# Kernel optimization log

Hardware: AMD Instinct MI355X
Metric: run time of the kernel (lower is better)

## Reference

```python
import jax, jax.numpy as jnp
import numpy as np

NEG_SLOPE = 0.2  # GATv2Conv default leaky_relu slope

def _ln(x, g, b, eps=1e-5):
    mu = jnp.mean(x, -1, keepdims=True)
    v = jnp.mean((x - mu) ** 2, -1, keepdims=True)
    return (x - mu) / jnp.sqrt(v + eps) * g + b

def _seg_softmax(s, seg, n):
    m = jax.ops.segment_max(s, seg, n)
    m = jnp.where(jnp.isfinite(m), m, 0.0)  # guard empty segments
    e = jnp.exp(s - m[seg])
    z = jax.ops.segment_sum(e, seg, n)
    return e / (z[seg] + 1e-16)

def _gatv2(x, src, dst, Wl, bl, Wr, br, att, bias, g, b):
    # GATv2Conv (concat=True) + dropout(noop, eval) + residual (dims match) + LN + ELU
    N = x.shape[0]
    H, D = att.shape
    xl = (x @ Wl + bl).reshape(N, H, D)   # source transform
    xr = (x @ Wr + br).reshape(N, H, D)   # target transform
    e = jax.nn.leaky_relu(xl[src] + xr[dst], NEG_SLOPE)  # [E,H,D]
    sc = jnp.einsum('ehd,hd->eh', e, att)
    alpha = _seg_softmax(sc, dst, N)      # softmax over incoming edges per dst
    out = jax.ops.segment_sum(alpha[..., None] * xl[src], dst, N).reshape(N, H * D) + bias
    out = out + x                          # residual: in_dim == heads*out_dim
    return jax.nn.elu(_ln(out, g, b))

def _lstm(x, w_ih, w_hh, b_ih, b_hh):
    # torch LSTM gate order: i, f, g, o
    Hn = w_hh.shape[1]
    def step(carry, xt):
        h, c = carry
        gates = xt @ w_ih.T + h @ w_hh.T + b_ih + b_hh
        i, f, gg, o = jnp.split(gates, 4, -1)
        c = jax.nn.sigmoid(f) * c + jax.nn.sigmoid(i) * jnp.tanh(gg)
        h = jax.nn.sigmoid(o) * jnp.tanh(c)
        return (h, c), h
    h0 = jnp.zeros((x.shape[0], Hn), x.dtype)
    _, hs = jax.lax.scan(step, (h0, h0), jnp.swapaxes(x, 0, 1))
    return jnp.swapaxes(hs, 0, 1)  # [N,T,Hn]

def setup_inputs():
    key = jax.random.key(0)
    N, T, F, Hd, Hh, L = 20000, 20, 64, 256, 4, 2
    E, S, ES = 640000, 64, 1024
    D = Hd // Hh
    ks = iter(jax.random.split(key, 90))
    def nrm(shape, scale):
        return jax.random.normal(next(ks), shape, jnp.float32) * scale
    sH = Hd ** -0.5
    inp = {}
    inp['x_stock'] = nrm((N, T, F), 1.0)
    inp['edge_index_stock'] = jax.random.randint(next(ks), (2, E), 0, N)
    inp['batch_stock'] = jnp.sort(jax.random.randint(next(ks), (N,), 0, S))
    inp['x_sector'] = nrm((S, Hd), 1.0)
    inp['edge_index_sector'] = jax.random.randint(next(ks), (2, ES), 0, S)
    inp['ln_feat_g'] = jnp.ones(F); inp['ln_feat_b'] = jnp.zeros(F)
    inp['w_ih0'] = nrm((4 * Hd, F), F ** -0.5); inp['w_hh0'] = nrm((4 * Hd, Hd), sH)
    inp['b_ih0'] = jnp.zeros(4 * Hd); inp['b_hh0'] = jnp.zeros(4 * Hd)
    inp['w_ih1'] = nrm((4 * Hd, Hd), sH); inp['w_hh1'] = nrm((4 * Hd, Hd), sH)
    inp['b_ih1'] = jnp.zeros(4 * Hd); inp['b_hh1'] = jnp.zeros(4 * Hd)
    inp['ln_t_g'] = jnp.ones(Hd); inp['ln_t_b'] = jnp.zeros(Hd)
    inp['W_in'] = nrm((Hd, Hd), sH); inp['b_in'] = jnp.zeros(Hd)
    for p in ('stock', 'sector'):
        inp[p + '_Wl'] = nrm((L, Hd, Hd), sH); inp[p + '_bl'] = jnp.zeros((L, Hd))
        inp[p + '_Wr'] = nrm((L, Hd, Hd), sH); inp[p + '_br'] = jnp.zeros((L, Hd))
        inp[p + '_att'] = nrm((L, Hh, D), sH); inp[p + '_bias'] = jnp.zeros((L, Hd))
        inp[p + '_g'] = jnp.ones((L, Hd)); inp[p + '_b'] = jnp.zeros((L, Hd))
    inp['Wa1'] = nrm((Hd, Hd // 2), sH); inp['ba1'] = jnp.zeros(Hd // 2)
    inp['Wa2'] = nrm((Hd // 2, 1), (Hd // 2) ** -0.5); inp['ba2'] = jnp.zeros(1)
    inp['Wf'] = nrm((2 * Hd, Hd), (2 * Hd) ** -0.5); inp['bf'] = jnp.zeros(Hd)
    inp['gf'] = jnp.ones(Hd); inp['bef'] = jnp.zeros(Hd)
    for t in ('regf', 'clff', 'rnkf'):
        inp['W_' + t] = nrm((Hd, Hd), sH); inp['b_' + t] = jnp.zeros(Hd)
        inp['g_' + t] = jnp.ones(Hd); inp['be_' + t] = jnp.zeros(Hd)
    h2, h4 = Hd // 2, Hd // 4
    inp['Wr1'] = nrm((Hd, h2), sH); inp['br1'] = jnp.zeros(h2)
    inp['Wr2'] = nrm((h2, h4), h2 ** -0.5); inp['br2'] = jnp.zeros(h4)
    inp['Wr3'] = nrm((h4, 1), h4 ** -0.5); inp['br3'] = jnp.zeros(1)
    inp['Wc1'] = nrm((Hd, h2), sH); inp['bc1'] = jnp.zeros(h2)
    inp['Wc2'] = nrm((h2, 2), h2 ** -0.5); inp['bc2'] = jnp.zeros(2)
    inp['Wk1'] = nrm((Hd, h2), sH); inp['bk1'] = jnp.zeros(h2)
    inp['Wk2'] = nrm((h2, 1), h2 ** -0.5); inp['bk2'] = jnp.zeros(1)
    return inp

def _forward(x_stock, x_sector, ln_feat_g, ln_feat_b, w_ih0, w_hh0, b_ih0, b_hh0,
             w_ih1, w_hh1, b_ih1, b_hh1, ln_t_g, ln_t_b, W_in, b_in,
             stock_Wl, stock_bl, stock_Wr, stock_br, stock_att, stock_bias, stock_g, stock_b,
             Wa1, ba1, Wa2, ba2,
             sector_Wl, sector_bl, sector_Wr, sector_br, sector_att, sector_bias, sector_g, sector_b,
             Wf, bf, gf, bef,
             W_regf, b_regf, g_regf, be_regf, W_clff, b_clff, g_clff, be_clff,
             W_rnkf, b_rnkf, g_rnkf, be_rnkf,
             Wr1, br1, Wr2, br2, Wr3, br3, Wc1, bc1, Wc2, bc2, Wk1, bk1, Wk2, bk2,
             edge_index_stock, batch_stock, edge_index_sector):
    N = x_stock.shape[0]
    S = x_sector.shape[0]  # x_sector is otherwise unused by the torch forward
    # feature_norm + 2-layer LSTM temporal encoder (eval mode: dropout off)
    x = _ln(x_stock, ln_feat_g, ln_feat_b)
    h = _lstm(x, w_ih0, w_hh0, b_ih0, b_hh0)
    h = _lstm(h, w_ih1, w_hh1, b_ih1, b_hh1)
    x = _ln(h[:, -1], ln_t_g, ln_t_b)
    x = x @ W_in + b_in
    # stock GAT stack (with self loops, as in add_self_loops=True)
    sl = jnp.arange(N)
    src = jnp.concatenate([edge_index_stock[0], sl])
    dst = jnp.concatenate([edge_index_stock[1], sl])
    for l in range(stock_Wl.shape[0]):
        x = _gatv2(x, src, dst, stock_Wl[l], stock_bl[l], stock_Wr[l], stock_br[l],
                   stock_att[l], stock_bias[l], stock_g[l], stock_b[l])
    # attention pooling: per-sector softmax then mean pool of weighted feats
    sc = (jnp.tanh(x @ Wa1 + ba1) @ Wa2 + ba2)[:, 0]
    w = _seg_softmax(sc, batch_stock, S)
    cnt = jax.ops.segment_sum(jnp.ones(N, x.dtype), batch_stock, S)
    se = jax.ops.segment_sum(w[:, None] * x, batch_stock, S) / jnp.maximum(cnt, 1.0)[:, None]
    # sector GAT stack
    ssl = jnp.arange(S)
    ssrc = jnp.concatenate([edge_index_sector[0], ssl])
    sdst = jnp.concatenate([edge_index_sector[1], ssl])
    for l in range(sector_Wl.shape[0]):
        se = _gatv2(se, ssrc, sdst, sector_Wl[l], sector_bl[l], sector_Wr[l], sector_br[l],
                    sector_att[l], sector_bias[l], sector_g[l], sector_b[l])
    comb = jnp.concatenate([x, se[batch_stock]], -1)
    c = jax.nn.elu(_ln(comb @ Wf + bf, gf, bef))  # fusion_proj
    rf = jax.nn.relu(_ln(c @ W_regf + b_regf, g_regf, be_regf))
    cf = jax.nn.relu(_ln(c @ W_clff + b_clff, g_clff, be_clff))
    kf = jax.nn.relu(_ln(c @ W_rnkf + b_rnkf, g_rnkf, be_rnkf))
    ret = jnp.tanh(jax.nn.relu(jax.nn.relu(rf @ Wr1 + br1) @ Wr2 + br2) @ Wr3 + br3)[:, 0] * 0.1
    mov = jax.nn.relu(cf @ Wc1 + bc1) @ Wc2 + bc2
    rnk = jax.nn.sigmoid(jax.nn.relu(kf @ Wk1 + bk1) @ Wk2 + bk2)[:, 0]
    return ret, mov, rnk, c

def reference(x_stock, x_sector, ln_feat_g, ln_feat_b, w_ih0, w_hh0, b_ih0, b_hh0,
              w_ih1, w_hh1, b_ih1, b_hh1, ln_t_g, ln_t_b, W_in, b_in,
              stock_Wl, stock_bl, stock_Wr, stock_br, stock_att, stock_bias, stock_g, stock_b,
              Wa1, ba1, Wa2, ba2,
              sector_Wl, sector_bl, sector_Wr, sector_br, sector_att, sector_bias, sector_g, sector_b,
              Wf, bf, gf, bef,
              W_regf, b_regf, g_regf, be_regf, W_clff, b_clff, g_clff, be_clff,
              W_rnkf, b_rnkf, g_rnkf, be_rnkf,
              Wr1, br1, Wr2, br2, Wr3, br3, Wc1, bc1, Wc2, bc2, Wk1, bk1, Wk2, bk2,
              edge_index_stock, batch_stock, edge_index_sector):
    return _forward(x_stock, x_sector, ln_feat_g, ln_feat_b, w_ih0, w_hh0, b_ih0, b_hh0,
                    w_ih1, w_hh1, b_ih1, b_hh1, ln_t_g, ln_t_b, W_in, b_in,
                    stock_Wl, stock_bl, stock_Wr, stock_br, stock_att, stock_bias, stock_g, stock_b,
                    Wa1, ba1, Wa2, ba2,
                    sector_Wl, sector_bl, sector_Wr, sector_br, sector_att, sector_bias, sector_g, sector_b,
                    Wf, bf, gf, bef,
                    W_regf, b_regf, g_regf, be_regf, W_clff, b_clff, g_clff, be_clff,
                    W_rnkf, b_rnkf, g_rnkf, be_rnkf,
                    Wr1, br1, Wr2, br2, Wr3, br3, Wc1, bc1, Wc2, bc2, Wk1, bk1, Wk2, bk2,
                    edge_index_stock, batch_stock, edge_index_sector)
```

## Files before the change

kernel.cpp:

```cpp
#include <hip/hip_runtime.h>
#include <stdint.h>

static constexpr int TT = 20;
static constexpr int FF = 64;
static constexpr int HD = 256;

enum { ACT_NONE = 0, ACT_RELU = 1, ACT_TANH = 2 };

typedef __attribute__((ext_vector_type(8))) short short8;
typedef __attribute__((ext_vector_type(4))) float f32x4;

static __device__ __forceinline__ float sigf(float x) { return 1.f / (1.f + expf(-x)); }

static __device__ __forceinline__ ushort f2bf(float f) {
  uint32_t u = __float_as_uint(f);
  return (ushort)((u + 0x7fffu + ((u >> 16) & 1u)) >> 16);
}
static __device__ __forceinline__ float bf2f(ushort u) {
  return __uint_as_float(((uint32_t)u) << 16);
}
static __device__ __forceinline__ void gl16(const void* g, void* l) {
  __builtin_amdgcn_global_load_lds(
      (const __attribute__((address_space(1))) uint32_t*)g,
      (__attribute__((address_space(3))) uint32_t*)l, 16, 0, 0);
}

__global__ void k_lncvt(const float* __restrict__ x, const float* __restrict__ g,
                        const float* __restrict__ b, ushort* __restrict__ y, int rows) {
  int row = blockIdx.x * 4 + (threadIdx.x >> 6);
  int lane = threadIdx.x & 63;
  if (row >= rows) return;
  float v = x[(size_t)row * 64 + lane];
  float s = v, s2 = v * v;
  for (int o = 32; o; o >>= 1) { s += __shfl_xor(s, o); s2 += __shfl_xor(s2, o); }
  float m = s * (1.f / 64.f);
  float var = s2 * (1.f / 64.f) - m * m;
  float rs = rsqrtf(var + 1e-5f);
  y[(size_t)row * 64 + lane] = f2bf((v - m) * rs * g[lane] + b[lane]);
}

__global__ void k_build_wtile(const float* __restrict__ w_ih, const float* __restrict__ w_hh,
                              ushort* __restrict__ wt, int KI, int KT) {
  int total = 8 * KT * 512;
  for (int idx = blockIdx.x * blockDim.x + threadIdx.x; idx < total;
       idx += gridDim.x * blockDim.x) {
    int nb = idx / (KT * 512);
    int rem = idx % (KT * 512);
    int kt = rem / 512;
    int q = rem % 512;
    int r = q >> 2, csw = q & 3;
    int ch = csw ^ ((r >> 1) & 3);
    int col = nb * 128 + r;
    int hdblk = col >> 6, gg = (col >> 4) & 3, hd = hdblk * 16 + (col & 15);
    int orow = gg * HD + hd;
    int k = kt * 32 + ch * 8;
    const float* src = (k < KI) ? (w_ih + (size_t)orow * KI + k)
                                : (w_hh + (size_t)orow * HD + (k - KI));
    ushort* dst = wt + (size_t)idx * 8;
#pragma unroll
    for (int j = 0; j < 8; j++) dst[j] = f2bf(src[j]);
  }
}

__global__ void k_build_bcp(const float* __restrict__ bi, const float* __restrict__ bh,
                            float* __restrict__ bcp) {
  int col = blockIdx.x * blockDim.x + threadIdx.x;
  if (col >= 1024) return;
  int hdblk = col >> 6, gg = (col >> 4) & 3, hd = hdblk * 16 + (col & 15);
  int orow = gg * HD + hd;
  bcp[col] = bi[orow] + bh[orow];
}

__global__ void k_build_btile(const float* __restrict__ B, ushort* __restrict__ bt,
                              int K, int Nn, int NB) {
  int KTb = K / 32;
  int total = NB * KTb * 512;
  for (int idx = blockIdx.x * blockDim.x + threadIdx.x; idx < total;
       idx += gridDim.x * blockDim.x) {
    int nb = idx / (KTb * 512);
    int rem = idx % (KTb * 512);
    int kt = rem / 512;
    int q = rem % 512;
    int r = q >> 2, csw = q & 3;
    int ch = csw ^ ((r >> 1) & 3);
    int col = nb * 128 + r;
    int k = kt * 32 + ch * 8;
    ushort* dst = bt + (size_t)idx * 8;
#pragma unroll
    for (int j = 0; j < 8; j++)
      dst[j] = (col < Nn) ? f2bf(B[(size_t)(k + j) * Nn + col]) : (ushort)0;
  }
}

__global__ void k_cat2(const float* __restrict__ a, const float* __restrict__ b,
                       float* __restrict__ o) {
  int i = blockIdx.x * 256 + threadIdx.x;
  if (i < 256) o[i] = a[i];
  else if (i < 512) o[i] = b[i - 256];
}

template <int LAYER>
__device__ __forceinline__ void lstm_body(
    ushort* At, ushort* Bt,
    const ushort* __restrict__ a0, const ushort* __restrict__ a1,
    const ushort* __restrict__ wt, const float* __restrict__ bcp,
    float* __restrict__ cst, ushort* __restrict__ hnext, int M, int t) {
  constexpr int K = (LAYER == 0) ? 320 : 512;
  constexpr int KT = K / 32;
  constexpr int SEG0 = (LAYER == 0) ? 64 : 256;
  constexpr int LDA0 = (LAYER == 0) ? (TT * FF) : HD;
  const int tid = threadIdx.x;
  const int lane = tid & 63, wid = tid >> 6;
  const int wr = wid >> 1, wc = wid & 1;
  const int m0 = blockIdx.x * 128;
  const int nb = blockIdx.y;
  const int a0t = (LAYER == 0) ? t * FF : 0;

  f32x4 acc[4][4];
#pragma unroll
  for (int i = 0; i < 4; i++)
#pragma unroll
    for (int j = 0; j < 4; j++) acc[i][j] = (f32x4){0.f, 0.f, 0.f, 0.f};

  int rown[2], chn[2];
#pragma unroll
  for (int e = 0; e < 2; e++) {
    int q = e * 256 + tid;
    int r = q >> 2, csw = q & 3;
    rown[e] = r;
    chn[e] = csw ^ ((r >> 1) & 3);
  }
  const size_t wtbase = (size_t)nb * KT * 512;

  for (int kt = 0; kt < KT; ++kt) {
    __syncthreads();
    const int k0 = kt * 32;
#pragma unroll
    for (int e = 0; e < 2; e++) {
      int q = e * 256 + tid;
      int r = rown[e];
      int kg = k0 + chn[e] * 8;
      int grow = m0 + r;
      grow = (grow < M) ? grow : (M - 1);
      const ushort* src = (kg < SEG0)
                              ? (a0 + (size_t)grow * LDA0 + a0t + kg)
                              : (a1 + (size_t)grow * HD + (kg - SEG0));
      gl16(src, &At[q * 8]);
      gl16(wt + (wtbase + (size_t)kt * 512 + q) * 8, &Bt[q * 8]);
    }
    __syncthreads();
    short8 af[4], bfr[4];
#pragma unroll
    for (int i = 0; i < 4; i++) {
      int rA = wr * 64 + i * 16 + (lane & 15);
      int swa = (lane >> 4) ^ ((rA >> 1) & 3);
      af[i] = *(const short8*)&At[rA * 32 + swa * 8];
      int rB = wc * 64 + i * 16 + (lane & 15);
      int swb = (lane >> 4) ^ ((rB >> 1) & 3);
      bfr[i] = *(const short8*)&Bt[rB * 32 + swb * 8];
    }
#pragma unroll
    for (int i = 0; i < 4; i++)
#pragma unroll
      for (int j = 0; j < 4; j++)
        acc[i][j] = __builtin_amdgcn_mfma_f32_16x16x32_bf16(af[i], bfr[j], acc[i][j], 0, 0, 0);
  }
  const int hdlo = lane & 15;
  const int rb = (lane >> 4) * 4;
  const int colb = nb * 128 + wc * 64;
  const float bI = bcp[colb + hdlo];
  const float bF = bcp[colb + 16 + hdlo];
  const float bG = bcp[colb + 32 + hdlo];
  const float bO = bcp[colb + 48 + hdlo];
  const int hd = (nb * 2 + wc) * 16 + hdlo;
#pragma unroll
  for (int i = 0; i < 4; i++) {
#pragma unroll
    for (int r = 0; r < 4; r++) {
      int row = m0 + wr * 64 + i * 16 + rb + r;
      if (row >= M) continue;
      float gi = acc[i][0][r] + bI;
      float gf = acc[i][1][r] + bF;
      float gg = acc[i][2][r] + bG;
      float go = acc[i][3][r] + bO;
      size_t ix = (size_t)row * HD + hd;
      float c = sigf(gf) * cst[ix] + sigf(gi) * tanhf(gg);
      cst[ix] = c;
      hnext[ix] = f2bf(sigf(go) * tanhf(c));
    }
  }
}

template <int LAYER>
__global__ __launch_bounds__(256) void k_lstm_single(
    const ushort* __restrict__ a0, const ushort* __restrict__ a1,
    const ushort* __restrict__ wt, const float* __restrict__ bcp,
    float* __restrict__ cst, ushort* __restrict__ hnext, int M, int t) {
  __shared__ ushort At[128 * 32];
  __shared__ ushort Bt[128 * 32];
  lstm_body<LAYER>(At, Bt, a0, a1, wt, bcp, cst, hnext, M, t);
}

__global__ __launch_bounds__(256) void k_lstm_pair(
    const ushort* __restrict__ xln,
    const ushort* __restrict__ h0cur, const ushort* __restrict__ h1cur,
    const ushort* __restrict__ wt0, const float* __restrict__ bcp0,
    const ushort* __restrict__ wt1, const float* __restrict__ bcp1,
    float* __restrict__ c0, float* __restrict__ c1,
    ushort* __restrict__ h0next, ushort* __restrict__ h1next,
    int M, int tnext) {
  __shared__ ushort At[128 * 32];
  __shared__ ushort Bt[128 * 32];
  if (blockIdx.z == 0)
    lstm_body<1>(At, Bt, h0cur, h1cur, wt1, bcp1, c1, h1next, M, 0);
  else
    lstm_body<0>(At, Bt, xln, h0cur, wt0, bcp0, c0, h0next, M, tnext);
}

template <bool BF16OUT>
__global__ __launch_bounds__(256) void k_gemm_mfma(
    const float* __restrict__ A, int lda, const ushort* __restrict__ BtG,
    const float* __restrict__ bias, void* __restrict__ Cv, int ldc,
    int M, int Nn, int K, int act) {
  const int KTb = K / 32;
  __shared__ ushort At[128 * 32];
  __shared__ ushort Bts[128 * 32];
  const int tid = threadIdx.x;
  const int lane = tid & 63, wid = tid >> 6;
  const int wr = wid >> 1, wc = wid & 1;
  const int m0 = blockIdx.x * 128;
  const int nb = blockIdx.y;

  f32x4 acc[4][4];
#pragma unroll
  for (int i = 0; i < 4; i++)
#pragma unroll
    for (int j = 0; j < 4; j++) acc[i][j] = (f32x4){0.f, 0.f, 0.f, 0.f};

  const size_t btbase = (size_t)nb * KTb * 512;

  for (int kt = 0; kt < KTb; ++kt) {
    __syncthreads();
    const int k0 = kt * 32;
#pragma unroll
    for (int e = 0; e < 2; e++) {
      int q = e * 256 + tid;
      int r = q >> 2, csw = q & 3;
      int ch = csw ^ ((r >> 1) & 3);
      int row = m0 + r;
      row = (row < M) ? row : (M - 1);
      const float* src = A + (size_t)row * lda + k0 + ch * 8;
      float4 f0 = *(const float4*)src;
      float4 f1 = *(const float4*)(src + 4);
      short8 s;
      s[0] = (short)f2bf(f0.x); s[1] = (short)f2bf(f0.y);
      s[2] = (short)f2bf(f0.z); s[3] = (short)f2bf(f0.w);
      s[4] = (short)f2bf(f1.x); s[5] = (short)f2bf(f1.y);
      s[6] = (short)f2bf(f1.z); s[7] = (short)f2bf(f1.w);
      *(short8*)&At[q * 8] = s;
      gl16(BtG + (btbase + (size_t)kt * 512 + q) * 8, &Bts[q * 8]);
    }
    __syncthreads();
    short8 af[4], bfr[4];
#pragma unroll
    for (int i = 0; i < 4; i++) {
      int rA = wr * 64 + i * 16 + (lane & 15);
      int swa = (lane >> 4) ^ ((rA >> 1) & 3);
      af[i] = *(const short8*)&At[rA * 32 + swa * 8];
      int rB = wc * 64 + i * 16 + (lane & 15);
      int swb = (lane >> 4) ^ ((rB >> 1) & 3);
      bfr[i] = *(const short8*)&Bts[rB * 32 + swb * 8];
    }
#pragma unroll
    for (int i = 0; i < 4; i++)
#pragma unroll
      for (int j = 0; j < 4; j++)
        acc[i][j] = __builtin_amdgcn_mfma_f32_16x16x32_bf16(af[i], bfr[j], acc[i][j], 0, 0, 0);
  }
  const int rb = (lane >> 4) * 4;
  const int cl = lane & 15;
#pragma unroll
  for (int i = 0; i < 4; i++) {
#pragma unroll
    for (int j = 0; j < 4; j++) {
      int col = nb * 128 + wc * 64 + j * 16 + cl;
      if (col >= Nn) continue;
      float bv = bias[col];
#pragma unroll
      for (int r = 0; r < 4; r++) {
        int row = m0 + wr * 64 + i * 16 + rb + r;
        if (row >= M) continue;
        float v = acc[i][j][r] + bv;
        if (act == ACT_RELU) v = fmaxf(v, 0.f);
        else if (act == ACT_TANH) v = tanhf(v);
        if (BF16OUT) ((ushort*)Cv)[(size_t)row * ldc + col] = f2bf(v);
        else ((float*)Cv)[(size_t)row * ldc + col] = v;
      }
    }
  }
}

__global__ __launch_bounds__(256) void k_ln_rows(
    const float* __restrict__ in, float* __restrict__ out,
    const float* __restrict__ g, const float* __restrict__ b, int rows, int act) {
  int row = blockIdx.x;
  if (row >= rows) return;
  int tid = threadIdx.x, lane = tid & 63, wv = tid >> 6;
  float v = in[(size_t)row * HD + tid];
  float s = v, s2 = v * v;
  for (int o = 32; o; o >>= 1) { s += __shfl_xor(s, o); s2 += __shfl_xor(s2, o); }
  __shared__ float ws1[4], ws2[4];
  if (lane == 0) { ws1[wv] = s; ws2[wv] = s2; }
  __syncthreads();
  float S1 = ws1[0] + ws1[1] + ws1[2] + ws1[3];
  float S2 = ws2[0] + ws2[1] + ws2[2] + ws2[3];
  float m = S1 * (1.f / 256.f);
  float var = S2 * (1.f / 256.f) - m * m;
  float r = rsqrtf(var + 1e-5f);
  float y = (v - m) * r * g[tid] + b[tid];
  if (act == 1) y = fmaxf(y, 0.f);
  else if (act == 2) y = (y > 0.f) ? y : (expf(y) - 1.f);
  out[(size_t)row * HD + tid] = y;
}

__global__ __launch_bounds__(256) void k_ln_rows_b16(
    const ushort* __restrict__ in, float* __restrict__ out,
    const float* __restrict__ g, const float* __restrict__ b, int rows, int act) {
  int row = blockIdx.x;
  if (row >= rows) return;
  int tid = threadIdx.x, lane = tid & 63, wv = tid >> 6;
  float v = bf2f(in[(size_t)row * HD + tid]);
  float s = v, s2 = v * v;
  for (int o = 32; o; o >>= 1) { s += __shfl_xor(s, o); s2 += __shfl_xor(s2, o); }
  __shared__ float ws1[4], ws2[4];
  if (lane == 0) { ws1[wv] = s; ws2[wv] = s2; }
  __syncthreads();
  float S1 = ws1[0] + ws1[1] + ws1[2] + ws1[3];
  float S2 = ws2[0] + ws2[1] + ws2[2] + ws2[3];
  float m = S1 * (1.f / 256.f);
  float var = S2 * (1.f / 256.f) - m * m;
  float r = rsqrtf(var + 1e-5f);
  float y = (v - m) * r * g[tid] + b[tid];
  if (act == 1) y = fmaxf(y, 0.f);
  else if (act == 2) y = (y > 0.f) ? y : (expf(y) - 1.f);
  out[(size_t)row * HD + tid] = y;
}

__global__ void k_hist_edges(const int* __restrict__ dst, int E, int n, int* __restrict__ cnt) {
  int tot = E + n;
  for (int i = blockIdx.x * blockDim.x + threadIdx.x; i < tot; i += gridDim.x * blockDim.x) {
    int d = (i < E) ? dst[i] : (i - E);
    atomicAdd(&cnt[d], 1);
  }
}

__global__ void k_scan1(const int* __restrict__ cnt, int* __restrict__ ptr,
                        int* __restrict__ bsum, int n) {
  __shared__ int sm[1024];
  int tid = threadIdx.x, i = blockIdx.x * 1024 + tid;
  int v = (i < n) ? cnt[i] : 0;
  sm[tid] = v;
  __syncthreads();
  for (int off = 1; off < 1024; off <<= 1) {
    int t = (tid >= off) ? sm[tid - off] : 0;
    __syncthreads();
    sm[tid] += t;
    __syncthreads();
  }
  if (i < n) ptr[i] = sm[tid] - v;
  if (tid == 1023) bsum[blockIdx.x] = sm[1023];
}

__global__ void k_scan2(int* __restrict__ bsum, int nb) {
  __shared__ int sm[256];
  int tid = threadIdx.x;
  int v = (tid < nb) ? bsum[tid] : 0;
  sm[tid] = v;
  __syncthreads();
  for (int off = 1; off < 256; off <<= 1) {
    int t = (tid >= off) ? sm[tid - off] : 0;
    __syncthreads();
    sm[tid] += t;
    __syncthreads();
  }
  if (tid < nb) bsum[tid] = sm[tid] - v;
  if (tid == 0) bsum[nb] = sm[255];
}

__global__ void k_scan3(int* __restrict__ ptr, const int* __restrict__ bsum, int n, int nb) {
  int i = blockIdx.x * blockDim.x + threadIdx.x;
  if (i < n) ptr[i] += bsum[i >> 10];
  if (i == n) ptr[n] = bsum[nb];
}

__global__ void k_scatter_edges(const int* __restrict__ src, const int* __restrict__ dst,
                                int E, int n, const int* __restrict__ rowptr,
                                int* __restrict__ fill, int* __restrict__ esrc) {
  int tot = E + n;
  for (int i = blockIdx.x * blockDim.x + threadIdx.x; i < tot; i += gridDim.x * blockDim.x) {
    int d, s;
    if (i < E) { d = dst[i]; s = src[i]; } else { d = i - E; s = i - E; }
    int pos = rowptr[d] + atomicAdd(&fill[d], 1);
    esrc[pos] = s;
  }
}

__global__ void k_batch_bounds(const int* __restrict__ batch, int* __restrict__ bptr,
                               int n, int S) {
  int i = blockIdx.x * blockDim.x + threadIdx.x;
  if (i > n) return;
  if (i == 0) {
    int b0 = batch[0];
    for (int s = 0; s <= b0; s++) bptr[s] = 0;
  } else if (i == n) {
    int bl = batch[n - 1];
    for (int s = bl + 1; s <= S; s++) bptr[s] = n;
  } else {
    int a = batch[i - 1], b = batch[i];
    for (int s = a + 1; s <= b; s++) bptr[s] = i;
  }
}

__global__ __launch_bounds__(256) void k_gat_wave(
    const float* __restrict__ xin, const ushort* __restrict__ xlr,
    const int* __restrict__ rowptr, const int* __restrict__ esrc,
    const float* __restrict__ att, const float* __restrict__ bias,
    const float* __restrict__ lng, const float* __restrict__ lnb,
    float* __restrict__ xout, int n_nodes) {
  const int wid = threadIdx.x >> 6;
  const int nd = blockIdx.x * 4 + wid;
  if (nd >= n_nodes) return;
  const int lane = threadIdx.x & 63;
  const int eg = lane >> 4;
  const int dq = lane & 15;
  const int dbase = dq * 16;

  float xr16[16], at16[16];
  {
    const ushort* xr = xlr + (size_t)nd * 512 + 256 + dbase;
    short8 a = *(const short8*)xr;
    short8 b = *(const short8*)(xr + 8);
#pragma unroll
    for (int j = 0; j < 8; j++) { xr16[j] = bf2f((ushort)a[j]); xr16[8 + j] = bf2f((ushort)b[j]); }
    const float* ap = att + dbase;
#pragma unroll
    for (int j = 0; j < 16; j++) at16[j] = ap[j];
  }
  const int rs = rowptr[nd];
  const int deg = rowptr[nd + 1] - rs;

  float m = -3e38f, z = 0.f;
  float acc[16];
#pragma unroll
  for (int j = 0; j < 16; j++) acc[j] = 0.f;

  for (int p = eg; p < deg; p += 4) {
    int src = esrc[rs + p];
    const ushort* xl = xlr + (size_t)src * 512 + dbase;
    short8 a = *(const short8*)xl;
    short8 b = *(const short8*)(xl + 8);
    float xv[16];
#pragma unroll
    for (int j = 0; j < 8; j++) { xv[j] = bf2f((ushort)a[j]); xv[8 + j] = bf2f((ushort)b[j]); }
    float sc = 0.f;
#pragma unroll
    for (int j = 0; j < 16; j++) {
      float v = xv[j] + xr16[j];
      v = (v > 0.f) ? v : 0.2f * v;
      sc = fmaf(v, at16[j], sc);
    }
    sc += __shfl_xor(sc, 1);
    sc += __shfl_xor(sc, 2);
    if (sc > m + 8.f) {
      float r = __expf(m - sc);
      z *= r;
#pragma unroll
      for (int j = 0; j < 16; j++) acc[j] *= r;
      m = sc;
    }
    float w = __expf(sc - m);
    z += w;
#pragma unroll
    for (int j = 0; j < 16; j++) acc[j] = fmaf(w, xv[j], acc[j]);
  }
  float mt = fmaxf(m, __shfl_xor(m, 16));
  mt = fmaxf(mt, __shfl_xor(mt, 32));
  float r = __expf(m - mt);
  z *= r;
  z += __shfl_xor(z, 16);
  z += __shfl_xor(z, 32);
#pragma unroll
  for (int j = 0; j < 16; j++) {
    float a = acc[j] * r;
    a += __shfl_xor(a, 16);
    a += __shfl_xor(a, 32);
    acc[j] = a;
  }
  float zinv = 1.f / (z + 1e-16f);
  const float* xi = xin + (size_t)nd * 256 + dbase;
  const float* bp = bias + dbase;
  float v16[16];
  float s1 = 0.f, s2 = 0.f;
#pragma unroll
  for (int j = 0; j < 16; j++) {
    float v = acc[j] * zinv + bp[j] + xi[j];
    v16[j] = v;
    s1 += v;
    s2 += v * v;
  }
  for (int o = 32; o; o >>= 1) { s1 += __shfl_xor(s1, o); s2 += __shfl_xor(s2, o); }
  float mean = s1 * (1.f / 1024.f);
  float var = s2 * (1.f / 1024.f) - mean * mean;
  float rstd = rsqrtf(var + 1e-5f);
  const float* gp = lng + dbase + eg * 4;
  const float* bb = lnb + dbase + eg * 4;
  float4 o4;
#pragma unroll
  for (int jj = 0; jj < 4; jj++) {
    float y = (v16[eg * 4 + jj] - mean) * rstd * gp[jj] + bb[jj];
    y = (y > 0.f) ? y : (expf(y) - 1.f);
    (&o4.x)[jj] = y;
  }
  *(float4*)(xout + (size_t)nd * 256 + dbase + eg * 4) = o4;
}

__global__ void k_rowdot(const float* __restrict__ in, const float* __restrict__ W,
                         const float* __restrict__ bias, float* __restrict__ out,
                         int rows, int K, int OC, int act) {
  int row = blockIdx.x * 4 + (threadIdx.x >> 6);
  if (row >= rows) return;
  int lane = threadIdx.x & 63;
  for (int o = 0; o < OC; o++) {
    float s = 0.f;
    for (int k = lane; k < K; k += 64) s += in[(size_t)row * K + k] * W[(size_t)k * OC + o];
    for (int off = 32; off; off >>= 1) s += __shfl_xor(s, off);
    if (lane == 0) {
      float v = s + bias[o];
      if (act == 3) v = tanhf(v) * 0.1f;
      else if (act == 4) v = 1.f / (1.f + expf(-v));
      out[(size_t)row * OC + o] = v;
    }
  }
}

__global__ __launch_bounds__(256) void k_sector_pool(
    const float* __restrict__ x, const float* __restrict__ sc,
    const int* __restrict__ bptr, float* __restrict__ se, int S) {
  const int s = blockIdx.x, tid = threadIdx.x, lane = tid & 63, wv = tid >> 6;
  const int rs = bptr[s], re = bptr[s + 1];
  const int cnt = re - rs;
  __shared__ float r1[4], r2[4], wch[256];
  float mx = -3e38f;
  for (int i = rs + tid; i < re; i += 256) mx = fmaxf(mx, sc[i]);
  for (int o = 32; o; o >>= 1) mx = fmaxf(mx, __shfl_xor(mx, o));
  if (lane == 0) r1[wv] = mx;
  __syncthreads();
  float m = fmaxf(fmaxf(r1[0], r1[1]), fmaxf(r1[2], r1[3]));
  if (cnt == 0) m = 0.f;
  float z = 0.f;
  for (int i = rs + tid; i < re; i += 256) z += expf(sc[i] - m);
  for (int o = 32; o; o >>= 1) z += __shfl_xor(z, o);
  if (lane == 0) r2[wv] = z;
  __syncthreads();
  float zinv = 1.f / (r2[0] + r2[1] + r2[2] + r2[3] + 1e-16f);
  float acc = 0.f;
  for (int base = rs; base < re; base += 256) {
    int i = base + tid;
    wch[tid] = (i < re) ? expf(sc[i] - m) * zinv : 0.f;
    __syncthreads();
    int lim = re - base; if (lim > 256) lim = 256;
    for (int q = 0; q < lim; q++) acc += wch[q] * x[(size_t)(base + q) * HD + tid];
    __syncthreads();
  }
  se[(size_t)s * HD + tid] = acc / fmaxf((float)cnt, 1.f);
}

__global__ void k_comb(const float* __restrict__ x, const float* __restrict__ se,
                       const int* __restrict__ batch, float* __restrict__ comb, int n) {
  int total = n * 512;
  for (int i = blockIdx.x * blockDim.x + threadIdx.x; i < total; i += gridDim.x * blockDim.x) {
    int row = i >> 9, col = i & 511;
    comb[i] = (col < HD) ? x[(size_t)row * HD + col]
                         : se[(size_t)batch[row] * HD + (col - HD)];
  }
}

extern "C" void kernel_launch(void* const* d_in, const int* in_sizes, int n_in,
                              void* d_out, int out_size, void* d_ws, size_t ws_size,
                              hipStream_t stream) {
  const float* x_stock   = (const float*)d_in[0];
  const int*   ei_stock  = (const int*)d_in[1];
  const int*   batch     = (const int*)d_in[2];
  const int*   ei_sector = (const int*)d_in[4];
  const float* ln_feat_g = (const float*)d_in[5];
  const float* ln_feat_b = (const float*)d_in[6];
  const float* w_ih0 = (const float*)d_in[7];
  const float* w_hh0 = (const float*)d_in[8];
  const float* b_ih0 = (const float*)d_in[9];
  const float* b_hh0 = (const float*)d_in[10];
  const float* w_ih1 = (const float*)d_in[11];
  const float* w_hh1 = (const float*)d_in[12];
  const float* b_ih1 = (const float*)d_in[13];
  const float* b_hh1 = (const float*)d_in[14];
  const float* ln_t_g = (const float*)d_in[15];
  const float* ln_t_b = (const float*)d_in[16];
  const float* W_in = (const float*)d_in[17];
  const float* b_in = (const float*)d_in[18];
  const float* stock_Wl = (const float*)d_in[19];
  const float* stock_bl = (const float*)d_in[20];
  const float* stock_Wr = (const float*)d_in[21];
  const float* stock_br = (const float*)d_in[22];
  const float* stock_att = (const float*)d_in[23];
  const float* stock_bias = (const float*)d_in[24];
  const float* stock_g = (const float*)d_in[25];
  const float* stock_b = (const float*)d_in[26];
  const float* sector_Wl = (const float*)d_in[27];
  const float* sector_bl = (const float*)d_in[28];
  const float* sector_Wr = (const float*)d_in[29];
  const float* sector_br = (const float*)d_in[30];
  const float* sector_att = (const float*)d_in[31];
  const float* sector_bias = (const float*)d_in[32];
  const float* sector_g = (const float*)d_in[33];
  const float* sector_b = (const float*)d_in[34];
  const float* Wa1 = (const float*)d_in[35];
  const float* ba1 = (const float*)d_in[36];
  const float* Wa2 = (const float*)d_in[37];
  const float* ba2 = (const float*)d_in[38];
  const float* Wf  = (const float*)d_in[39];
  const float* bf  = (const float*)d_in[40];
  const float* gf  = (const float*)d_in[41];
  const float* bef = (const float*)d_in[42];
  const float* W_regf = (const float*)d_in[43];
  const float* b_regf = (const float*)d_in[44];
  const float* g_regf = (const float*)d_in[45];
  const float* be_regf = (const float*)d_in[46];
  const float* W_clff = (const float*)d_in[47];
  const float* b_clff = (const float*)d_in[48];
  const float* g_clff = (const float*)d_in[49];
  const float* be_clff = (const float*)d_in[50];
  const float* W_rnkf = (const float*)d_in[51];
  const float* b_rnkf = (const float*)d_in[52];
  const float* g_rnkf = (const float*)d_in[53];
  const float* be_rnkf = (const float*)d_in[54];
  const float* Wr1 = (const float*)d_in[55];
  const float* br1 = (const float*)d_in[56];
  const float* Wr2 = (const float*)d_in[57];
  const float* br2 = (const float*)d_in[58];
  const float* Wr3 = (const float*)d_in[59];
  const float* br3 = (const float*)d_in[60];
  const float* Wc1 = (const float*)d_in[61];
  const float* bc1 = (const float*)d_in[62];
  const float* Wc2 = (const float*)d_in[63];
  const float* bc2 = (const float*)d_in[64];
  const float* Wk1 = (const float*)d_in[65];
  const float* bk1 = (const float*)d_in[66];
  const float* Wk2 = (const float*)d_in[67];
  const float* bk2 = (const float*)d_in[68];

  const int N  = in_sizes[0] / (TT * FF);
  const int E  = in_sizes[1] / 2;
  const int S  = in_sizes[3] / HD;
  const int ES = in_sizes[4] / 2;
  const int Ep = E + N, ESp = ES + S;
  const int NT = N * TT;
  const int KT0 = 10, KT1 = 16;

  char* wsb = (char*)d_ws;
  size_t off = 0;
  auto alloc = [&](size_t bytes) -> char* {
    char* p = wsb + off;
    off += (bytes + 255) & ~(size_t)255;
    return p;
  };
  ushort* h0a = (ushort*)alloc((size_t)N * HD * 2);
  ushort* h1a = (ushort*)alloc((size_t)N * HD * 2);
  float*  c0  = (float*)alloc((size_t)N * HD * 4);
  float*  c1  = (float*)alloc((size_t)N * HD * 4);
  size_t zf_bytes = off;
  ushort* h0b = (ushort*)alloc((size_t)N * HD * 2);
  ushort* h1b = (ushort*)alloc((size_t)N * HD * 2);
  ushort* wt0 = (ushort*)alloc((size_t)8 * KT0 * 512 * 16);
  ushort* wt1 = (ushort*)alloc((size_t)8 * KT1 * 512 * 16);
  float* bcp0 = (float*)alloc(1024 * 4);
  float* bcp1 = (float*)alloc(1024 * 4);
  float* xA  = (float*)alloc((size_t)N * HD * 4);
  float* xB  = (float*)alloc((size_t)N * HD * 4);
  char*  xlr_raw = alloc((size_t)N * 512 * 4);
  float* scbuf = (float*)alloc((size_t)N * 128 * 4);
  char*  selr_raw = alloc((size_t)S * 512 * 4);
  float* seA  = (float*)alloc((size_t)S * HD * 4);
  float* seB  = (float*)alloc((size_t)S * HD * 4);
  float* scpool = (float*)alloc((size_t)N * 4);
  char* bigraw = alloc((size_t)N * TT * FF * 2);
  ushort* xln    = (ushort*)bigraw;
  float*  tmpY   = (float*)bigraw;
  float*  headbuf = (float*)(bigraw + (size_t)N * HD * 4);
  auto alloc_bt = [&](int K, int Nn) -> ushort* {
    int NB = (Nn + 127) / 128;
    return (ushort*)alloc((size_t)NB * (K / 32) * 512 * 16);
  };
  ushort* bt_Win  = alloc_bt(256, 256);
  ushort* bt_slr0 = alloc_bt(256, 512);
  ushort* bt_slr1 = alloc_bt(256, 512);
  ushort* bt_elr0 = alloc_bt(256, 512);
  ushort* bt_elr1 = alloc_bt(256, 512);
  ushort* bt_Wa1  = alloc_bt(256, 128);
  ushort* bt_Wf   = alloc_bt(512, 256);
  ushort* bt_Wreg = alloc_bt(256, 256);
  ushort* bt_Wclf = alloc_bt(256, 256);
  ushort* bt_Wrnk = alloc_bt(256, 256);
  ushort* bt_Wr1  = alloc_bt(256, 128);
  ushort* bt_Wr2  = alloc_bt(128, 64);
  ushort* bt_Wc1  = alloc_bt(256, 128);
  ushort* bt_Wk1  = alloc_bt(256, 128);
  float* bc_slr0 = (float*)alloc(512 * 4);
  float* bc_slr1 = (float*)alloc(512 * 4);
  float* bc_elr0 = (float*)alloc(512 * 4);
  float* bc_elr1 = (float*)alloc(512 * 4);
  size_t zi_start = off;
  int* cnt   = (int*)alloc((size_t)(N + 1) * 4);
  int* fill  = (int*)alloc((size_t)N * 4);
  int* cntS  = (int*)alloc((size_t)(S + 1) * 4);
  int* fillS = (int*)alloc((size_t)S * 4);
  size_t zi_bytes = off - zi_start;
  int* rowptr = (int*)alloc((size_t)(N + 1) * 4);
  int* esrc   = (int*)alloc((size_t)Ep * 4);
  int* rptrS  = (int*)alloc((size_t)(S + 1) * 4);
  int* esrcS  = (int*)alloc((size_t)ESp * 4);
  int* bptr   = (int*)alloc((size_t)(S + 1) * 4);
  int* bsum1  = (int*)alloc(64 * 4);
  int* bsum2  = (int*)alloc(64 * 4);

  ushort* xlr_b = (ushort*)xlr_raw;
  float*  comb  = (float*)xlr_raw;
  ushort* selr_b = (ushort*)selr_raw;
  float* hA   = scbuf;
  float* t128 = tmpY;
  float* t64  = tmpY + (size_t)N * 128;
  float* out_ret = (float*)d_out;
  float* out_mov = out_ret + N;
  float* out_rnk = out_ret + 3 * (size_t)N;
  float* out_c   = out_ret + 4 * (size_t)N;

  hipMemsetAsync(d_ws, 0, zf_bytes, stream);
  hipMemsetAsync(wsb + zi_start, 0, zi_bytes, stream);

  auto build_bt = [&](const float* W, ushort* bt, int K, int Nn) {
    int NB = (Nn + 127) / 128;
    int total = NB * (K / 32) * 512;
    k_build_btile<<<dim3((total + 255) / 256), dim3(256), 0, stream>>>(W, bt, K, Nn, NB);
  };
  auto gemm_f = [&](const float* A, int lda, const ushort* bt, const float* bias,
                    float* C, int ldc, int M, int Nn, int K, int act) {
    dim3 g((M + 127) / 128, (Nn + 127) / 128);
    k_gemm_mfma<false><<<g, dim3(256), 0, stream>>>(A, lda, bt, bias, C, ldc, M, Nn, K, act);
  };
  auto gemm_b = [&](const float* A, int lda, const ushort* bt, const float* bias,
                    ushort* C, int ldc, int M, int Nn, int K, int act) {
    dim3 g((M + 127) / 128, (Nn + 127) / 128);
    k_gemm_mfma<true><<<g, dim3(256), 0, stream>>>(A, lda, bt, bias, C, ldc, M, Nn, K, act);
  };
  const int TILE2 = 2 * 8 * 512 * 8;

  k_lncvt<<<dim3((NT + 3) / 4), dim3(256), 0, stream>>>(x_stock, ln_feat_g, ln_feat_b, xln, NT);
  k_build_wtile<<<dim3((8 * KT0 * 512 + 255) / 256), dim3(256), 0, stream>>>(w_ih0, w_hh0, wt0, FF, KT0);
  k_build_wtile<<<dim3((8 * KT1 * 512 + 255) / 256), dim3(256), 0, stream>>>(w_ih1, w_hh1, wt1, HD, KT1);
  k_build_bcp<<<dim3(4), dim3(256), 0, stream>>>(b_ih0, b_hh0, bcp0);
  k_build_bcp<<<dim3(4), dim3(256), 0, stream>>>(b_ih1, b_hh1, bcp1);
  build_bt(W_in, bt_Win, 256, 256);
  build_bt(stock_Wl, bt_slr0, 256, 256);
  build_bt(stock_Wr, bt_slr0 + TILE2, 256, 256);
  build_bt(stock_Wl + HD * HD, bt_slr1, 256, 256);
  build_bt(stock_Wr + HD * HD, bt_slr1 + TILE2, 256, 256);
  build_bt(sector_Wl, bt_elr0, 256, 256);
  build_bt(sector_Wr, bt_elr0 + TILE2, 256, 256);
  build_bt(sector_Wl + HD * HD, bt_elr1, 256, 256);
  build_bt(sector_Wr + HD * HD, bt_elr1 + TILE2, 256, 256);
  k_cat2<<<dim3(2), dim3(256), 0, stream>>>(stock_bl, stock_br, bc_slr0);
  k_cat2<<<dim3(2), dim3(256), 0, stream>>>(stock_bl + HD, stock_br + HD, bc_slr1);
  k_cat2<<<dim3(2), dim3(256), 0, stream>>>(sector_bl, sector_br, bc_elr0);
  k_cat2<<<dim3(2), dim3(256), 0, stream>>>(sector_bl + HD, sector_br + HD, bc_elr1);
  build_bt(Wa1, bt_Wa1, 256, 128);
  build_bt(Wf, bt_Wf, 512, 256);
  build_bt(W_regf, bt_Wreg, 256, 256);
  build_bt(W_clff, bt_Wclf, 256, 256);
  build_bt(W_rnkf, bt_Wrnk, 256, 256);
  build_bt(Wr1, bt_Wr1, 256, 128);
  build_bt(Wr2, bt_Wr2, 128, 64);
  build_bt(Wc1, bt_Wc1, 256, 128);
  build_bt(Wk1, bt_Wk1, 256, 128);

  {
    const int MB = (N + 127) / 128;
    ushort *h0c = h0a, *h0n = h0b, *h1c = h1a, *h1n = h1b;
    k_lstm_single<0><<<dim3(MB, 8), dim3(256), 0, stream>>>(xln, h0c, wt0, bcp0, c0, h0n, N, 0);
    { ushort* tp = h0c; h0c = h0n; h0n = tp; }
    for (int t = 0; t < TT - 1; t++) {
      k_lstm_pair<<<dim3(MB, 8, 2), dim3(256), 0, stream>>>(
          xln, h0c, h1c, wt0, bcp0, wt1, bcp1, c0, c1, h0n, h1n, N, t + 1);
      ushort* tp = h0c; h0c = h0n; h0n = tp;
      tp = h1c; h1c = h1n; h1n = tp;
    }
    k_lstm_single<1><<<dim3(MB, 8), dim3(256), 0, stream>>>(h0c, h1c, wt1, bcp1, c1, h1n, N, 0);
    k_ln_rows_b16<<<dim3(N), dim3(256), 0, stream>>>(h1n, tmpY, ln_t_g, ln_t_b, N, 0);
  }
  gemm_f(tmpY, HD, bt_Win, b_in, xA, HD, N, 256, 256, ACT_NONE);

  {
    int nb1 = (N + 1023) / 1024;
    k_hist_edges<<<dim3(2048), dim3(256), 0, stream>>>(ei_stock + E, E, N, cnt);
    k_scan1<<<dim3(nb1), dim3(1024), 0, stream>>>(cnt, rowptr, bsum1, N);
    k_scan2<<<dim3(1), dim3(256), 0, stream>>>(bsum1, nb1);
    k_scan3<<<dim3((N + 256) / 256), dim3(256), 0, stream>>>(rowptr, bsum1, N, nb1);
    k_scatter_edges<<<dim3(2048), dim3(256), 0, stream>>>(ei_stock, ei_stock + E, E, N,
                                                          rowptr, fill, esrc);
  }
  float* xc = xA; float* xn = xB;
  const ushort* btS[2] = {bt_slr0, bt_slr1};
  const float*  bcS[2] = {bc_slr0, bc_slr1};
  for (int l = 0; l < 2; l++) {
    const float* at = stock_att + (size_t)l * HD;
    const float* bi = stock_bias + (size_t)l * HD;
    const float* lg = stock_g + (size_t)l * HD;
    const float* lb = stock_b + (size_t)l * HD;
    gemm_b(xc, HD, btS[l], bcS[l], xlr_b, 512, N, 512, 256, ACT_NONE);
    k_gat_wave<<<dim3((N + 3) / 4), dim3(256), 0, stream>>>(xc, xlr_b, rowptr, esrc,
                                                            at, bi, lg, lb, xn, N);
    float* tp = xc; xc = xn; xn = tp;
  }
  gemm_f(xc, HD, bt_Wa1, ba1, hA, 128, N, 128, 256, ACT_TANH);
  k_rowdot<<<dim3((N + 3) / 4), dim3(256), 0, stream>>>(hA, Wa2, ba2, scpool, N, 128, 1, 0);
  k_batch_bounds<<<dim3((N + 256) / 256), dim3(256), 0, stream>>>(batch, bptr, N, S);
  k_sector_pool<<<dim3(S), dim3(256), 0, stream>>>(xc, scpool, bptr, seA, S);
  {
    int nb1 = (S + 1023) / 1024;
    k_hist_edges<<<dim3(64), dim3(256), 0, stream>>>(ei_sector + ES, ES, S, cntS);
    k_scan1<<<dim3(nb1), dim3(1024), 0, stream>>>(cntS, rptrS, bsum2, S);
    k_scan2<<<dim3(1), dim3(256), 0, stream>>>(bsum2, nb1);
    k_scan3<<<dim3((S + 256) / 256), dim3(256), 0, stream>>>(rptrS, bsum2, S, nb1);
    k_scatter_edges<<<dim3(64), dim3(256), 0, stream>>>(ei_sector, ei_sector + ES, ES, S,
                                                        rptrS, fillS, esrcS);
  }
  float* sec = seA; float* sen = seB;
  const ushort* btE[2] = {bt_elr0, bt_elr1};
  const float*  bcE[2] = {bc_elr0, bc_elr1};
  for (int l = 0; l < 2; l++) {
    const float* at = sector_att + (size_t)l * HD;
    const float* bi = sector_bias + (size_t)l * HD;
    const float* lg = sector_g + (size_t)l * HD;
    const float* lb = sector_b + (size_t)l * HD;
    gemm_b(sec, HD, btE[l], bcE[l], selr_b, 512, S, 512, 256, ACT_NONE);
    k_gat_wave<<<dim3((S + 3) / 4), dim3(256), 0, stream>>>(sec, selr_b, rptrS, esrcS,
                                                            at, bi, lg, lb, sen, S);
    float* tp = sec; sec = sen; sen = tp;
  }
  k_comb<<<dim3(4096), dim3(256), 0, stream>>>(xc, sec, batch, comb, N);
  gemm_f(comb, 512, bt_Wf, bf, tmpY, HD, N, 256, 512, ACT_NONE);
  k_ln_rows<<<dim3(N), dim3(256), 0, stream>>>(tmpY, out_c, gf, bef, N, 2);
  gemm_f(out_c, HD, bt_Wreg, b_regf, tmpY, HD, N, 256, 256, ACT_NONE);
  k_ln_rows<<<dim3(N), dim3(256), 0, stream>>>(tmpY, headbuf, g_regf, be_regf, N, 1);
  gemm_f(headbuf, HD, bt_Wr1, br1, t128, 128, N, 128, 256, ACT_RELU);
  gemm_f(t128, 128, bt_Wr2, br2, t64, 64, N, 64, 128, ACT_RELU);
  k_rowdot<<<dim3((N + 3) / 4), dim3(256), 0, stream>>>(t64, Wr3, br3, out_ret, N, 64, 1, 3);
  gemm_f(out_c, HD, bt_Wclf, b_clff, tmpY, HD, N, 256, 256, ACT_NONE);
  k_ln_rows<<<dim3(N), dim3(256), 0, stream>>>(tmpY, headbuf, g_clff, be_clff, N, 1);
  gemm_f(headbuf, HD, bt_Wc1, bc1, t128, 128, N, 128, 256, ACT_RELU);
  k_rowdot<<<dim3((N + 3) / 4), dim3(256), 0, stream>>>(t128, Wc2, bc2, out_mov, N, 128, 2, 0);
  gemm_f(out_c, HD, bt_Wrnk, b_rnkf, tmpY, HD, N, 256, 256, ACT_NONE);
  k_ln_rows<<<dim3(N), dim3(256), 0, stream>>>(tmpY, headbuf, g_rnkf, be_rnkf, N, 1);
  gemm_f(headbuf, HD, bt_Wk1, bk1, t128, 128, N, 128, 256, ACT_RELU);
  k_rowdot<<<dim3((N + 3) / 4), dim3(256), 0, stream>>>(t128, Wk2, bk2, out_rnk, N, 128, 1, 4);
}
```

Baseline: 3.071 ms.

## Widen LSTM gate tiles to 128x256 with 512-thread blocks

The LSTM step GEMM tile grows from 128x128 to 128x256 gate columns. Each block now runs 8 waves (2x4) and the grid's column dimension halves, and the weight tile layout is rebuilt to match. Each A tile (input/hidden rows) is now loaded once per 256 output columns instead of once per 128, halving redundant A traffic. The cost is more LDS per block and possibly lower occupancy or fewer blocks for latency hiding.

```diff
diff --git a/kernel.cpp b/kernel.cpp
--- a/kernel.cpp
+++ b/kernel.cpp
@@ -41,16 +41,16 @@
 
 __global__ void k_build_wtile(const float* __restrict__ w_ih, const float* __restrict__ w_hh,
                               ushort* __restrict__ wt, int KI, int KT) {
-  int total = 8 * KT * 512;
+  int total = 4 * KT * 1024;
   for (int idx = blockIdx.x * blockDim.x + threadIdx.x; idx < total;
        idx += gridDim.x * blockDim.x) {
-    int nb = idx / (KT * 512);
-    int rem = idx % (KT * 512);
-    int kt = rem / 512;
-    int q = rem % 512;
+    int nb = idx / (KT * 1024);
+    int rem = idx % (KT * 1024);
+    int kt = rem / 1024;
+    int q = rem % 1024;
     int r = q >> 2, csw = q & 3;
     int ch = csw ^ ((r >> 1) & 3);
-    int col = nb * 128 + r;
+    int col = nb * 256 + r;
     int hdblk = col >> 6, gg = (col >> 4) & 3, hd = hdblk * 16 + (col & 15);
     int orow = gg * HD + hd;
     int k = kt * 32 + ch * 8;
@@ -100,7 +100,7 @@
 }
 
 template <int LAYER>
-__device__ __forceinline__ void lstm_body(
+__device__ __forceinline__ void lstm_body8(
     ushort* At, ushort* Bt,
     const ushort* __restrict__ a0, const ushort* __restrict__ a1,
     const ushort* __restrict__ wt, const float* __restrict__ bcp,
@@ -111,7 +111,7 @@
   constexpr int LDA0 = (LAYER == 0) ? (TT * FF) : HD;
   const int tid = threadIdx.x;
   const int lane = tid & 63, wid = tid >> 6;
-  const int wr = wid >> 1, wc = wid & 1;
+  const int wr = wid >> 2, wc = wid & 3;
   const int m0 = blockIdx.x * 128;
   const int nb = blockIdx.y;
   const int a0t = (LAYER == 0) ? t * FF : 0;
@@ -122,31 +122,26 @@
 #pragma unroll
     for (int j = 0; j < 4; j++) acc[i][j] = (f32x4){0.f, 0.f, 0.f, 0.f};
 
-  int rown[2], chn[2];
-#pragma unroll
-  for (int e = 0; e < 2; e++) {
-    int q = e * 256 + tid;
-    int r = q >> 2, csw = q & 3;
-    rown[e] = r;
-    chn[e] = csw ^ ((r >> 1) & 3);
-  }
-  const size_t wtbase = (size_t)nb * KT * 512;
+  const int rA_ = tid >> 2, cswA = tid & 3;
+  const int chA = cswA ^ ((rA_ >> 1) & 3);
+  int growA = m0 + rA_;
+  growA = (growA < M) ? growA : (M - 1);
+  const size_t wtbase = (size_t)nb * KT * 1024;
 
   for (int kt = 0; kt < KT; ++kt) {
     __syncthreads();
     const int k0 = kt * 32;
+    {
+      int kg = k0 + chA * 8;
+      const ushort* src = (kg < SEG0)
+                              ? (a0 + (size_t)growA * LDA0 + a0t + kg)
+                              : (a1 + (size_t)growA * HD + (kg - SEG0));
+      gl16(src, &At[tid * 8]);
+    }
 #pragma unroll
     for (int e = 0; e < 2; e++) {
-      int q = e * 256 + tid;
-      int r = rown[e];
-      int kg = k0 + chn[e] * 8;
-      int grow = m0 + r;
-      grow = (grow < M) ? grow : (M - 1);
-      const ushort* src = (kg < SEG0)
-                              ? (a0 + (size_t)grow * LDA0 + a0t + kg)
-                              : (a1 + (size_t)grow * HD + (kg - SEG0));
-      gl16(src, &At[q * 8]);
-      gl16(wt + (wtbase + (size_t)kt * 512 + q) * 8, &Bt[q * 8]);
+      int q = e * 512 + tid;
+      gl16(wt + (wtbase + (size_t)kt * 1024 + q) * 8, &Bt[q * 8]);
     }
     __syncthreads();
     short8 af[4], bfr[4];
@@ -167,12 +162,12 @@
   }
   const int hdlo = lane & 15;
   const int rb = (lane >> 4) * 4;
-  const int colb = nb * 128 + wc * 64;
+  const int colb = nb * 256 + wc * 64;
   const float bI = bcp[colb + hdlo];
   const float bF = bcp[colb + 16 + hdlo];
   const float bG = bcp[colb + 32 + hdlo];
   const float bO = bcp[colb + 48 + hdlo];
-  const int hd = (nb * 2 + wc) * 16 + hdlo;
+  const int hd = (nb * 4 + wc) * 16 + hdlo;
 #pragma unroll
   for (int i = 0; i < 4; i++) {
 #pragma unroll
@@ -192,16 +187,16 @@
 }
 
 template <int LAYER>
-__global__ __launch_bounds__(256) void k_lstm_single(
+__global__ __launch_bounds__(512) void k_lstm_single(
     const ushort* __restrict__ a0, const ushort* __restrict__ a1,
     const ushort* __restrict__ wt, const float* __restrict__ bcp,
     float* __restrict__ cst, ushort* __restrict__ hnext, int M, int t) {
   __shared__ ushort At[128 * 32];
-  __shared__ ushort Bt[128 * 32];
-  lstm_body<LAYER>(At, Bt, a0, a1, wt, bcp, cst, hnext, M, t);
-}
-
-__global__ __launch_bounds__(256) void k_lstm_pair(
+  __shared__ ushort Bt[256 * 32];
+  lstm_body8<LAYER>(At, Bt, a0, a1, wt, bcp, cst, hnext, M, t);
+}
+
+__global__ __launch_bounds__(512) void k_lstm_pair(
     const ushort* __restrict__ xln,
     const ushort* __restrict__ h0cur, const ushort* __restrict__ h1cur,
     const ushort* __restrict__ wt0, const float* __restrict__ bcp0,
@@ -210,11 +205,11 @@
     ushort* __restrict__ h0next, ushort* __restrict__ h1next,
     int M, int tnext) {
   __shared__ ushort At[128 * 32];
-  __shared__ ushort Bt[128 * 32];
+  __shared__ ushort Bt[256 * 32];
   if (blockIdx.z == 0)
-    lstm_body<1>(At, Bt, h0cur, h1cur, wt1, bcp1, c1, h1next, M, 0);
+    lstm_body8<1>(At, Bt, h0cur, h1cur, wt1, bcp1, c1, h1next, M, 0);
   else
-    lstm_body<0>(At, Bt, xln, h0cur, wt0, bcp0, c0, h0next, M, tnext);
+    lstm_body8<0>(At, Bt, xln, h0cur, wt0, bcp0, c0, h0next, M, tnext);
 }
 
 template <bool BF16OUT>
@@ -679,8 +674,8 @@
   size_t zf_bytes = off;
   ushort* h0b = (ushort*)alloc((size_t)N * HD * 2);
   ushort* h1b = (ushort*)alloc((size_t)N * HD * 2);
-  ushort* wt0 = (ushort*)alloc((size_t)8 * KT0 * 512 * 16);
-  ushort* wt1 = (ushort*)alloc((size_t)8 * KT1 * 512 * 16);
+  ushort* wt0 = (ushort*)alloc((size_t)4 * KT0 * 1024 * 16);
+  ushort* wt1 = (ushort*)alloc((size_t)4 * KT1 * 1024 * 16);
   float* bcp0 = (float*)alloc(1024 * 4);
   float* bcp1 = (float*)alloc(1024 * 4);
   float* xA  = (float*)alloc((size_t)N * HD * 4);
@@ -763,8 +758,8 @@
   const int TILE2 = 2 * 8 * 512 * 8;
 
   k_lncvt<<<dim3((NT + 3) / 4), dim3(256), 0, stream>>>(x_stock, ln_feat_g, ln_feat_b, xln, NT);
-  k_build_wtile<<<dim3((8 * KT0 * 512 + 255) / 256), dim3(256), 0, stream>>>(w_ih0, w_hh0, wt0, FF, KT0);
-  k_build_wtile<<<dim3((8 * KT1 * 512 + 255) / 256), dim3(256), 0, stream>>>(w_ih1, w_hh1, wt1, HD, KT1);
+  k_build_wtile<<<dim3((4 * KT0 * 1024 + 255) / 256), dim3(256), 0, stream>>>(w_ih0, w_hh0, wt0, FF, KT0);
+  k_build_wtile<<<dim3((4 * KT1 * 1024 + 255) / 256), dim3(256), 0, stream>>>(w_ih1, w_hh1, wt1, HD, KT1);
   k_build_bcp<<<dim3(4), dim3(256), 0, stream>>>(b_ih0, b_hh0, bcp0);
   k_build_bcp<<<dim3(4), dim3(256), 0, stream>>>(b_ih1, b_hh1, bcp1);
   build_bt(W_in, bt_Win, 256, 256);
@@ -793,15 +788,15 @@
   {
     const int MB = (N + 127) / 128;
     ushort *h0c = h0a, *h0n = h0b, *h1c = h1a, *h1n = h1b;
-    k_lstm_single<0><<<dim3(MB, 8), dim3(256), 0, stream>>>(xln, h0c, wt0, bcp0, c0, h0n, N, 0);
+    k_lstm_single<0><<<dim3(MB, 4), dim3(512), 0, stream>>>(xln, h0c, wt0, bcp0, c0, h0n, N, 0);
     { ushort* tp = h0c; h0c = h0n; h0n = tp; }
     for (int t = 0; t < TT - 1; t++) {
-      k_lstm_pair<<<dim3(MB, 8, 2), dim3(256), 0, stream>>>(
+      k_lstm_pair<<<dim3(MB, 4, 2), dim3(512), 0, stream>>>(
           xln, h0c, h1c, wt0, bcp0, wt1, bcp1, c0, c1, h0n, h1n, N, t + 1);
       ushort* tp = h0c; h0c = h0n; h0n = tp;
       tp = h1c; h1c = h1n; h1n = tp;
     }
-    k_lstm_single<1><<<dim3(MB, 8), dim3(256), 0, stream>>>(h0c, h1c, wt1, bcp1, c1, h1n, N, 0);
+    k_lstm_single<1><<<dim3(MB, 4), dim3(512), 0, stream>>>(h0c, h1c, wt1, bcp1, c1, h1n, N, 0);
     k_ln_rows_b16<<<dim3(N), dim3(256), 0, stream>>>(h1n, tmpY, ln_t_g, ln_t_b, N, 0);
   }
   gemm_f(tmpY, HD, bt_Win, b_in, xA, HD, N, 256, 256, ACT_NONE);
```

New measurement: 2.627 ms. 1.17x faster.
